# Kernel optimization log

Hardware: AMD Instinct MI355X
Metric: run time of the kernel (lower is better)

## Reference

```python
import jax, jax.numpy as jnp
import numpy as np

B, T, N, D, H = 4, 8, 128, 256, 8
DH = D // H
SH_HID = 16
NUM_FEATS = 3
NUM_COEFF = 4  # l=0 (1) + l=1 (3)
Y0_CONST = 0.28209479177387814   # 1/(2*sqrt(pi)), e3nn 'integral' norm
Y1_CONST = 0.4886025119029199    # sqrt(3/(4*pi))


def setup_inputs() -> dict:
    key = jax.random.key(0)
    ks = jax.random.split(key, 16)
    rn = lambda k, shape, s=1.0: jax.random.normal(k, shape, dtype=jnp.float32) * s
    return {
        "x_0": rn(ks[0], (B, T, N, D)),
        "v_0": rn(ks[1], (B, T, N, D)),
        "concatenated_features": rn(ks[2], (B, T, N, D)),
        "q_data": rn(ks[3], (B, T, N, D)),
        "mask": jnp.ones((B, 1, N, 1), dtype=bool),
        "Wq": rn(ks[4], (D, D), 0.02), "bq": jnp.zeros((D,), jnp.float32),
        "Wkv": rn(ks[5], (NUM_FEATS, D, 2 * D), 0.02),
        "bkv": jnp.zeros((NUM_FEATS, 2 * D), jnp.float32),
        "Wo": rn(ks[6], (D, D), 0.02), "bo": jnp.zeros((D,), jnp.float32),
        "feature_weights": rn(ks[7], (NUM_FEATS,), 0.1),
        "attention_denom": jnp.full((H,), float(DH), dtype=jnp.float32),
        "sh_W1": rn(ks[8], (NUM_COEFF, SH_HID), 0.3), "sh_b1": jnp.zeros((SH_HID,), jnp.float32),
        "sh_W2": rn(ks[9], (SH_HID, SH_HID), 0.3), "sh_b2": jnp.zeros((SH_HID,), jnp.float32),
        "sh_W3": rn(ks[10], (SH_HID, H), 0.3), "sh_b3": jnp.zeros((H,), jnp.float32),
    }


def _rope(t, mask, T_, N_):
    # t: [B,H,S,dh]; time-only RoPE, groups of N_ nodes share a timestep. offset=0.
    B_, H_, S, dh = t.shape
    half = dh // 2
    freqs = 1.0 / (1000.0 ** (2.0 * jnp.arange(half, dtype=jnp.float32) / dh))  # [half]
    pos = jnp.repeat(jnp.arange(T_, dtype=jnp.float32), N_)  # [S]
    angle = pos[:, None] * freqs[None, :]  # [S, half]
    mask_seq = jnp.broadcast_to(mask, (B_, T_, N_, 1)).reshape(B_, 1, S, 1)
    cos_t = jnp.where(mask_seq, jnp.cos(angle)[None, None], 1.0)  # [B,1,S,half]
    sin_t = jnp.where(mask_seq, jnp.sin(angle)[None, None], 0.0)
    t1, t2 = t[..., 0::2], t[..., 1::2]
    return jnp.stack([t1 * cos_t - t2 * sin_t, t1 * sin_t + t2 * cos_t], axis=-1).reshape(t.shape)


def _sh_bias(coords, W1, b1, W2, b2, W3, b3):
    # coords: [B,S,3] -> bias [B,H,S,S]
    rel = coords[:, :, None, :] - coords[:, None, :, :]  # [B,S,S,3]
    norm = jnp.sqrt(jnp.sum(rel * rel, axis=-1, keepdims=True))
    u = rel / (norm + 1e-6)
    Y0 = jnp.full(u.shape[:-1] + (1,), Y0_CONST, dtype=u.dtype)
    Y1 = Y1_CONST * u[..., jnp.array([1, 2, 0])]  # e3nn l=1 order (y,z,x)
    sh = jnp.concatenate([Y0, Y1], axis=-1)  # [B,S,S,4]
    h = jax.nn.silu(sh @ W1 + b1)
    h = jax.nn.silu(h @ W2 + b2)
    bias = h @ W3 + b3  # [B,S,S,H]
    return jnp.transpose(bias, (0, 3, 1, 2))


def reference(x_0, v_0, concatenated_features, q_data, mask,
              Wq, bq, Wkv, bkv, Wo, bo, feature_weights, attention_denom,
              sh_W1, sh_b1, sh_W2, sh_b2, sh_W3, sh_b3):
    B_, T_, N_, D_ = q_data.shape
    S = T_ * N_
    H_ = attention_denom.shape[0]
    dh = D_ // H_

    q = (q_data.reshape(B_, S, D_) @ Wq + bq).reshape(B_, S, H_, dh).transpose(0, 2, 1, 3)
    q = _rope(q, mask, T_, N_)

    coords = x_0[..., :3].reshape(B_, S, 3)
    bias = _sh_bias(coords, sh_W1, sh_b1, sh_W2, sh_b2, sh_W3, sh_b3)  # [B,H,S,S]

    key_mask = jnp.broadcast_to(mask, (B_, T_, N_, 1)).reshape(B_, 1, 1, S)
    gates = jax.nn.softmax(feature_weights)

    out_sum = jnp.zeros_like(q)
    for i, feat in enumerate((x_0, v_0, concatenated_features)):
        kv = feat.reshape(B_, S, D_) @ Wkv[i] + bkv[i]  # [B,S,2D]
        k = kv[..., :D_].reshape(B_, S, H_, dh).transpose(0, 2, 1, 3)
        v = kv[..., D_:].reshape(B_, S, H_, dh).transpose(0, 2, 1, 3)
        k = _rope(k, mask, T_, N_)
        scores = jnp.einsum('bhqd,bhkd->bhqk', q, k) / attention_denom[None, :, None, None]
        scores = scores + bias
        scores = jnp.where(key_mask, scores, -1e9)
        attn = jax.nn.softmax(scores, axis=-1)
        out_sum = out_sum + gates[i] * jnp.einsum('bhqk,bhkd->bhqd', attn, v)

    out = out_sum.transpose(0, 2, 1, 3).reshape(B_, S, D_) @ Wo + bo  # [B,S,D]
    return out.reshape(B_ * T_, N_, D_)
```

## Files before the change

### kernel.cpp

```cpp
#include <hip/hip_runtime.h>
#include <hip/hip_bf16.h>
#include <math.h>


typedef __bf16 bf16;
typedef __attribute__((ext_vector_type(8))) __bf16 bf16x8;
typedef __attribute__((ext_vector_type(4))) __bf16 bf16x4;
typedef __attribute__((ext_vector_type(4))) float  f32x4;

#define MFMA16(a,b,c) __builtin_amdgcn_mfma_f32_16x16x32_bf16((a),(b),(c),0,0,0)
#define FRCP(x) __builtin_amdgcn_rcpf(x)

__device__ __forceinline__ unsigned pk2(float a, float b){
  bf16 x = (bf16)a, y = (bf16)b;
  unsigned short ux = __builtin_bit_cast(unsigned short, x);
  unsigned short uy = __builtin_bit_cast(unsigned short, y);
  return (unsigned)ux | ((unsigned)uy << 16);
}

__global__ __launch_bounds__(256) void proj_kernel(
    const float* __restrict__ x0, const float* __restrict__ v0,
    const float* __restrict__ cf, const float* __restrict__ qd,
    const float* __restrict__ Wq, const float* __restrict__ bq,
    const float* __restrict__ Wkv, const float* __restrict__ bkv,
    const float* __restrict__ dn,
    bf16* __restrict__ Qb, bf16* __restrict__ Kb, bf16* __restrict__ Vtb)
{
  const int mtc = blockIdx.x;
  const int znt = blockIdx.y;
  int z, nt;
  if (znt < 4){ z = 0; nt = znt; } else { z = 1 + ((znt-4)>>3); nt = (znt-4)&7; }

  const float* A; const float* W; const float* bias; int ldw;
  if (z == 0){ A = qd; W = Wq; bias = bq; ldw = 256; }
  else {
    A = (z==1) ? x0 : (z==2) ? v0 : cf;
    W = Wkv + (size_t)(z-1)*256*512;
    bias = bkv + (size_t)(z-1)*512;
    ldw = 512;
  }

  __shared__ alignas(16) bf16 lds_w[64*264];
  __shared__ alignas(16) bf16 ostg[4][1152];
  const int t  = threadIdx.x;
  const int n0 = nt*64;

  {
    int c4 = t & 15, kr = t >> 4;
    #pragma unroll
    for (int i=0;i<16;i++){
      int k = kr + i*16;
      float4 v = *(const float4*)(W + (size_t)k*ldw + n0 + c4*4);
      lds_w[(c4*4+0)*264 + k] = (bf16)v.x;
      lds_w[(c4*4+1)*264 + k] = (bf16)v.y;
      lds_w[(c4*4+2)*264 + k] = (bf16)v.z;
      lds_w[(c4*4+3)*264 + k] = (bf16)v.w;
    }
  }
  __syncthreads();

  const int w = t>>6, lane = t&63, lrow = lane&15, g = lane>>4;
  const f32x4 zf = {0.f,0.f,0.f,0.f};
  const bool isV = (z>0) && (nt>=4);

  const float Cln = 0.43172239f;
  const float fr_e = __expf(-Cln * (float)(lrow>>1));
  const float fr_o = __expf(-Cln * (float)(8 + (lrow>>1)));
  float rs0 = 1.f, rs1 = 1.f;
  if (z==0){ rs0 = 1.f/dn[(nt*2)&7]; rs1 = 1.f/dn[(nt*2+1)&7]; }

  for (int mi=0; mi<4; mi++){
    const int mt = mtc*4 + mi;
    const float* Arow = A + (size_t)(mt*64 + w*16 + lrow)*256;

    f32x4 acc[4] = {zf,zf,zf,zf};
    #pragma unroll
    for (int ks=0;ks<8;ks++){
      float4 a0 = *(const float4*)(Arow + ks*32 + g*8);
      float4 a1 = *(const float4*)(Arow + ks*32 + g*8 + 4);
      bf16x8 af = {(bf16)a0.x,(bf16)a0.y,(bf16)a0.z,(bf16)a0.w,
                   (bf16)a1.x,(bf16)a1.y,(bf16)a1.z,(bf16)a1.w};
      #pragma unroll
      for (int n4=0;n4<4;n4++){
        bf16x8 bb = *(const bf16x8*)(lds_w + (n4*16+lrow)*264 + ks*32 + g*8);
        acc[n4] = MFMA16(af, bb, acc[n4]);
      }
    }

    if (!isV){
      const float tpos = (float)((mt>>1)&7);
      float ae = tpos*fr_e, ao = tpos*fr_o;
      float cs_e = __cosf(ae), sn_e = __sinf(ae);
      float cs_o = __cosf(ao), sn_o = __sinf(ao);
      #pragma unroll
      for (int n4=0;n4<4;n4++){
        int gcol = n0 + n4*16 + lrow;
        float bv = bias[gcol];
        float cs = (n4&1)? cs_o : cs_e;
        float sn = (n4&1)? sn_o : sn_e;
        float rs = (n4>>1)? rs1 : rs0;
        #pragma unroll
        for (int rr=0;rr<4;rr++){
          float v = acc[n4][rr] + bv;
          float p = __shfl_xor(v, 1);
          float o = (lrow&1) ? (p*sn + v*cs) : (v*cs - p*sn);
          o *= rs;
          ostg[w][(g*4+rr)*72 + n4*16 + lrow] = (bf16)o;
        }
      }
      asm volatile("s_waitcnt lgkmcnt(0)" ::: "memory");
      int row = lane>>2, c8 = lane&3;
      int srow = mt*64 + w*16 + row;
      int bb = srow>>10, s = srow&1023;
      #pragma unroll
      for (int hh=0; hh<2; hh++){
        bf16x8 val = *(const bf16x8*)(ostg[w] + row*72 + hh*32 + c8*8);
        int h = (nt*2 + hh)&7;
        bf16* dst = (z==0) ? (Qb + ((size_t)(bb*8+h)*1024 + s)*32 + c8*8)
                           : (Kb + ((size_t)(((z-1)*4+bb)*8+h)*1024 + s)*32 + c8*8);
        *(bf16x8*)dst = val;
      }
    } else {
      #pragma unroll
      for (int n4=0;n4<4;n4++){
        int gcol = n0 + n4*16 + lrow;
        float bv = bias[gcol];
        int hd = gcol - 256; int h = hd>>5, d = hd&31;
        int grow0 = mt*64 + w*16 + g*4;
        int bb = grow0>>10, s0 = grow0&1023;
        int s0p = (s0 & ~31) | (((s0>>2)&3)<<3) | (((s0>>4)&1)<<2);
        bf16x4 pk;
        #pragma unroll
        for (int rr=0;rr<4;rr++) pk[rr] = (bf16)(acc[n4][rr] + bv);
        *(bf16x4*)(Vtb + (((size_t)((z-1)*4+bb)*8 + h)*32 + d)*1024 + s0p) = pk;
      }
    }
  }
}

__global__ __launch_bounds__(512, 2) void attn_kernel(
    const bf16* __restrict__ Qb, const bf16* __restrict__ Kb, const bf16* __restrict__ Vtb,
    const float* __restrict__ x0, const float* __restrict__ fw,
    const float* __restrict__ W1, const float* __restrict__ b1,
    const float* __restrict__ W2, const float* __restrict__ b2,
    const float* __restrict__ W3, const float* __restrict__ b3,
    const float* __restrict__ Wo, const float* __restrict__ bo,
    float* __restrict__ out)
{
  const int bid = blockIdx.x;
  const int xcd = bid & 7;
  const int b   = xcd >> 1;
  const int qt  = (xcd & 1)*32 + (bid >> 3);
  const int q0  = qt*16;
  const int t = threadIdx.x, w = t>>6, lane = t&63, lrow = lane&15, g = lane>>4;

  __shared__ float smem[11776];
  float* ckA = smem;
  bf16* biasT0 = (bf16*)(smem + 3072);

  bf16x8 w1f, w2f, w3f;
  #pragma unroll
  for (int j=0;j<8;j++){
    w1f[j] = (g==0 && j<4)   ? (bf16)W1[j*16 + lrow]       : (bf16)0.f;
    w2f[j] = (j<4)           ? (bf16)W2[(4*g+j)*16 + lrow] : (bf16)0.f;
    w3f[j] = (j<4 && lrow<8) ? (bf16)W3[(4*g+j)*8 + lrow]  : (bf16)0.f;
  }
  float b1r[4], b2r[4], b3r[4];
  #pragma unroll
  for (int rr=0;rr<4;rr++){
    b1r[rr] = b1[g*4+rr];
    b2r[rr] = b2[g*4+rr];
    b3r[rr] = (g<2) ? b3[g*4+rr] : 0.f;
  }

  float f0=fw[0], f1=fw[1], f2=fw[2];
  float fm = fmaxf(f0, fmaxf(f1,f2));
  float e0=__expf(f0-fm), e1=__expf(f1-fm), e2=__expf(f2-fm);
  float ei = FRCP(e0+e1+e2);
  float gate[3] = {e0*ei, e1*ei, e2*ei};

  bf16x8 qf = *(const bf16x8*)(Qb + (((size_t)(b*8+w)*1024) + q0 + lrow)*32 + g*8);

  #pragma unroll
  for (int u=0;u<2;u++){
    int key = u*512 + t;
    const float* src = x0 + ((size_t)b*1024 + key)*256;
    ckA[key*3+0] = src[0]; ckA[key*3+1] = src[1]; ckA[key*3+2] = src[2];
  }
  __syncthreads();
  const float cqx = ckA[(q0+lrow)*3+0], cqy = ckA[(q0+lrow)*3+1], cqz = ckA[(q0+lrow)*3+2];

  auto MLP = [&](int kt_){
    const int k0 = kt_*64;
    bf16* bT = biasT0 + (kt_&1)*8704;
    const f32x4 zf = {0.f,0.f,0.f,0.f};
    #pragma unroll
    for (int m8=0;m8<8;m8++){
      const int m = w*8 + m8;
      float rx = cqx - ckA[(k0+m)*3+0];
      float ry = cqy - ckA[(k0+m)*3+1];
      float rz = cqz - ckA[(k0+m)*3+2];
      float inv = FRCP(__builtin_amdgcn_sqrtf(rx*rx+ry*ry+rz*rz) + 1e-6f);
      bf16x8 shf;
      #pragma unroll
      for (int j=0;j<8;j++) shf[j] = (bf16)0.f;
      if (g==0){
        shf[0] = (bf16)0.28209479177387814f;
        shf[1] = (bf16)(0.4886025119029199f*ry*inv);
        shf[2] = (bf16)(0.4886025119029199f*rz*inv);
        shf[3] = (bf16)(0.4886025119029199f*rx*inv);
      }
      f32x4 c1 = MFMA16(w1f, shf, zf);
      bf16x8 h1f;
      #pragma unroll
      for (int rr=0;rr<4;rr++){
        float hv = c1[rr] + b1r[rr];
        hv = hv * FRCP(1.f + __expf(-hv));
        bf16 hb = (bf16)hv;
        h1f[rr] = hb; h1f[rr+4] = hb;
      }
      f32x4 c2 = MFMA16(w2f, h1f, zf);
      bf16x8 h2f;
      #pragma unroll
      for (int rr=0;rr<4;rr++){
        float hv = c2[rr] + b2r[rr];
        hv = hv * FRCP(1.f + __expf(-hv));
        bf16 hb = (bf16)hv;
        h2f[rr] = hb; h2f[rr+4] = hb;
      }
      f32x4 c3 = MFMA16(w3f, h2f, zf);
      if (g < 2){
        #pragma unroll
        for (int rr=0;rr<4;rr++)
          bT[((g*4+rr)*64 + m)*17 + lrow] = (bf16)(c3[rr] + b3r[rr]);
      }
    }
  };

  float l_run[3] = {0.f,0.f,0.f};
  const f32x4 zf = {0.f,0.f,0.f,0.f};
  f32x4 acc[3][2];
  #pragma unroll
  for (int i=0;i<3;i++){ acc[i][0] = zf; acc[i][1] = zf; }

  MLP(0);
  __syncthreads();

  for (int kt=0;kt<16;kt++){
    const int k0 = kt*64;

    bf16x8 kpre[3][4], vpre[3][2][2];
    #pragma unroll
    for (int i=0;i<3;i++){
      const bf16* Kbase = Kb + ((size_t)(i*4+b)*8 + w)*1024*32;
      #pragma unroll
      for (int k16=0;k16<4;k16++)
        kpre[i][k16] = *(const bf16x8*)(Kbase + (size_t)(k0 + k16*16 + lrow)*32 + g*8);
      const bf16* Vbase = Vtb + ((size_t)(i*4+b)*8 + w)*32*1024;
      #pragma unroll
      for (int dt=0;dt<2;dt++){
        vpre[i][dt][0] = *(const bf16x8*)(Vbase + (size_t)(dt*16+lrow)*1024 + k0      + g*8);
        vpre[i][dt][1] = *(const bf16x8*)(Vbase + (size_t)(dt*16+lrow)*1024 + k0 + 32 + g*8);
      }
    }
    __builtin_amdgcn_sched_barrier(0);

    const bf16* bTr = biasT0 + (kt&1)*8704;
    float bias_r[4][4];
    #pragma unroll
    for (int k16=0;k16<4;k16++)
      #pragma unroll
      for (int rr=0;rr<4;rr++)
        bias_r[k16][rr] = (float)bTr[(w*64 + k16*16 + g*4 + rr)*17 + lrow];

    if (kt < 15) MLP(kt+1);

    #pragma unroll
    for (int i=0;i<3;i++){
      float p[4][4];
      float lp[4];
      #pragma unroll
      for (int k16=0;k16<4;k16++){
        f32x4 sc = MFMA16(kpre[i][k16], qf, zf);
        float s0 = 0.f;
        #pragma unroll
        for (int rr=0;rr<4;rr++){
          float pv = __expf(sc[rr] + bias_r[k16][rr]);
          p[k16][rr] = pv;
          s0 += pv;
        }
        lp[k16] = s0;
      }
      l_run[i] += (lp[0]+lp[1]) + (lp[2]+lp[3]);
      bf16x8 pf0, pf1;
      #pragma unroll
      for (int j=0;j<8;j++){
        pf0[j] = (bf16)p[(j>>2)][j&3];
        pf1[j] = (bf16)p[2+(j>>2)][j&3];
      }
      #pragma unroll
      for (int dt=0;dt<2;dt++){
        acc[i][dt] = MFMA16(vpre[i][dt][0], pf0, acc[i][dt]);
        acc[i][dt] = MFMA16(vpre[i][dt][1], pf1, acc[i][dt]);
      }
    }
    __syncthreads();
  }

  float linv[3];
  #pragma unroll
  for (int i=0;i<3;i++){
    float l = l_run[i];
    l += __shfl_xor(l, 16);
    l += __shfl_xor(l, 32);
    linv[i] = gate[i]*FRCP(l);
  }
  f32x4 o[2];
  #pragma unroll
  for (int dt=0;dt<2;dt++)
    #pragma unroll
    for (int rr=0;rr<4;rr++)
      o[dt][rr] = acc[0][dt][rr]*linv[0] + acc[1][dt][rr]*linv[1] + acc[2][dt][rr]*linv[2];

  unsigned* osTp = (unsigned*)smem;
  __syncthreads();
  #pragma unroll
  for (int dt=0;dt<2;dt++){
    int pb = w*16 + dt*8 + g*2;
    osTp[(pb+0)*17 + lrow] = pk2(o[dt][0], o[dt][1]);
    osTp[(pb+1)*17 + lrow] = pk2(o[dt][2], o[dt][3]);
  }
  __syncthreads();

  #pragma unroll
  for (int nt2=0;nt2<2;nt2++){
    const int n0 = w*32 + nt2*16;
    f32x4 c = zf;
    #pragma unroll
    for (int kb=0;kb<8;kb++){
      bf16x8 af;
      #pragma unroll
      for (int j=0;j<8;j++)
        af[j] = (bf16)Wo[(size_t)(kb*32 + g*8 + j)*256 + n0 + lrow];
      union { unsigned u[4]; bf16x8 v; } bu;
      #pragma unroll
      for (int jj=0;jj<4;jj++)
        bu.u[jj] = osTp[(kb*16 + g*4 + jj)*17 + lrow];
      c = MFMA16(af, bu.v, c);
    }
    #pragma unroll
    for (int rr=0;rr<4;rr++){
      int n = n0 + g*4 + rr;
      out[(size_t)(b*1024 + q0 + lrow)*256 + n] = c[rr] + bo[n];
    }
  }
}

extern "C" void kernel_launch(void* const* d_in, const int* in_sizes, int n_in,
                              void* d_out, int out_size, void* d_ws, size_t ws_size,
                              hipStream_t stream)
{
  (void)in_sizes; (void)n_in; (void)out_size; (void)ws_size;
  const float* x0 = (const float*)d_in[0];
  const float* v0 = (const float*)d_in[1];
  const float* cf = (const float*)d_in[2];
  const float* qd = (const float*)d_in[3];
  const float* Wq = (const float*)d_in[5];
  const float* bq = (const float*)d_in[6];
  const float* Wkv= (const float*)d_in[7];
  const float* bkv= (const float*)d_in[8];
  const float* Wo = (const float*)d_in[9];
  const float* bo = (const float*)d_in[10];
  const float* fw = (const float*)d_in[11];
  const float* dn = (const float*)d_in[12];
  const float* W1 = (const float*)d_in[13];
  const float* b1 = (const float*)d_in[14];
  const float* W2 = (const float*)d_in[15];
  const float* b2 = (const float*)d_in[16];
  const float* W3 = (const float*)d_in[17];
  const float* b3 = (const float*)d_in[18];

  const size_t nQ = (size_t)4*8*1024*32;
  const size_t nK = (size_t)3*4*8*1024*32;
  bf16*  Qb   = (bf16*)d_ws;
  bf16*  Kb   = Qb + nQ;
  bf16*  Vtb  = Kb + nK;
  float* outp = (float*)d_out;

  hipLaunchKernelGGL(proj_kernel, dim3(16,28), dim3(256), 0, stream,
                     x0, v0, cf, qd, Wq, bq, Wkv, bkv, dn, Qb, Kb, Vtb);
  hipLaunchKernelGGL(attn_kernel, dim3(256), dim3(512), 0, stream,
                     Qb, Kb, Vtb, x0, fw, W1,b1,W2,b2,W3,b3, Wo, bo, outp);
}
```

Measured before the change: 240.3 us.

## Split attention key range across two wave groups in 1024-thread blocks

The attention block grows from 512 to 1024 threads. Two groups of 8 waves each process half of the 1024 keys, and their partial accumulators and row sums are merged through shared memory before the output projection, which now uses all 16 waves. K/V register prefetch before the sched barrier is dropped in favour of loads inline with the MFMAs. This raises per-CU parallelism and halves the serial key loop, at the cost of more shared memory, extra barriers and a merge step, and may expose load latency now that prefetching is gone.

After: 315.1 us. +31.1%, slower.

```diff
diff --git a/kernel.cpp b/kernel.cpp
--- a/kernel.cpp
+++ b/kernel.cpp
@@ -138,7 +138,7 @@
   }
 }
 
-__global__ __launch_bounds__(512, 2) void attn_kernel(
+__global__ __launch_bounds__(1024, 4) void attn_kernel(
     const bf16* __restrict__ Qb, const bf16* __restrict__ Kb, const bf16* __restrict__ Vtb,
     const float* __restrict__ x0, const float* __restrict__ fw,
     const float* __restrict__ W1, const float* __restrict__ b1,
@@ -152,11 +152,14 @@
   const int b   = xcd >> 1;
   const int qt  = (xcd & 1)*32 + (bid >> 3);
   const int q0  = qt*16;
-  const int t = threadIdx.x, w = t>>6, lane = t&63, lrow = lane&15, g = lane>>4;
-
-  __shared__ float smem[11776];
+  const int t = threadIdx.x;
+  const int w16 = t>>6, split = w16>>3, w = w16&7;
+  const int lane = t&63, lrow = lane&15, g = lane>>4;
+  const int kbase = split*512;
+
+  __shared__ float smem[20480];
   float* ckA = smem;
-  bf16* biasT0 = (bf16*)(smem + 3072);
+  bf16* bgrp = (bf16*)(smem + 3072) + split*17408;
 
   bf16x8 w1f, w2f, w3f;
   #pragma unroll
@@ -181,18 +184,16 @@
 
   bf16x8 qf = *(const bf16x8*)(Qb + (((size_t)(b*8+w)*1024) + q0 + lrow)*32 + g*8);
 
-  #pragma unroll
-  for (int u=0;u<2;u++){
-    int key = u*512 + t;
-    const float* src = x0 + ((size_t)b*1024 + key)*256;
-    ckA[key*3+0] = src[0]; ckA[key*3+1] = src[1]; ckA[key*3+2] = src[2];
+  {
+    const float* src = x0 + ((size_t)b*1024 + t)*256;
+    ckA[t*3+0] = src[0]; ckA[t*3+1] = src[1]; ckA[t*3+2] = src[2];
   }
   __syncthreads();
   const float cqx = ckA[(q0+lrow)*3+0], cqy = ckA[(q0+lrow)*3+1], cqz = ckA[(q0+lrow)*3+2];
 
   auto MLP = [&](int kt_){
-    const int k0 = kt_*64;
-    bf16* bT = biasT0 + (kt_&1)*8704;
+    const int k0 = kbase + kt_*64;
+    bf16* bT = bgrp + (kt_&1)*8704;
     const f32x4 zf = {0.f,0.f,0.f,0.f};
     #pragma unroll
     for (int m8=0;m8<8;m8++){
@@ -246,42 +247,28 @@
   MLP(0);
   __syncthreads();
 
-  for (int kt=0;kt<16;kt++){
-    const int k0 = kt*64;
-
-    bf16x8 kpre[3][4], vpre[3][2][2];
+  for (int kt=0;kt<8;kt++){
+    const int kg = kbase + kt*64;
+
+    const bf16* bTr = bgrp + (kt&1)*8704;
+    float bias_r[4][4];
+    #pragma unroll
+    for (int k16=0;k16<4;k16++)
+      #pragma unroll
+      for (int rr=0;rr<4;rr++)
+        bias_r[k16][rr] = (float)bTr[(w*64 + k16*16 + g*4 + rr)*17 + lrow];
+
+    if (kt < 7) MLP(kt+1);
+
     #pragma unroll
     for (int i=0;i<3;i++){
       const bf16* Kbase = Kb + ((size_t)(i*4+b)*8 + w)*1024*32;
-      #pragma unroll
-      for (int k16=0;k16<4;k16++)
-        kpre[i][k16] = *(const bf16x8*)(Kbase + (size_t)(k0 + k16*16 + lrow)*32 + g*8);
-      const bf16* Vbase = Vtb + ((size_t)(i*4+b)*8 + w)*32*1024;
-      #pragma unroll
-      for (int dt=0;dt<2;dt++){
-        vpre[i][dt][0] = *(const bf16x8*)(Vbase + (size_t)(dt*16+lrow)*1024 + k0      + g*8);
-        vpre[i][dt][1] = *(const bf16x8*)(Vbase + (size_t)(dt*16+lrow)*1024 + k0 + 32 + g*8);
-      }
-    }
-    __builtin_amdgcn_sched_barrier(0);
-
-    const bf16* bTr = biasT0 + (kt&1)*8704;
-    float bias_r[4][4];
-    #pragma unroll
-    for (int k16=0;k16<4;k16++)
-      #pragma unroll
-      for (int rr=0;rr<4;rr++)
-        bias_r[k16][rr] = (float)bTr[(w*64 + k16*16 + g*4 + rr)*17 + lrow];
-
-    if (kt < 15) MLP(kt+1);
-
-    #pragma unroll
-    for (int i=0;i<3;i++){
       float p[4][4];
       float lp[4];
       #pragma unroll
       for (int k16=0;k16<4;k16++){
-        f32x4 sc = MFMA16(kpre[i][k16], qf, zf);
+        bf16x8 kf = *(const bf16x8*)(Kbase + (size_t)(kg + k16*16 + lrow)*32 + g*8);
+        f32x4 sc = MFMA16(kf, qf, zf);
         float s0 = 0.f;
         #pragma unroll
         for (int rr=0;rr<4;rr++){
@@ -298,43 +285,71 @@
         pf0[j] = (bf16)p[(j>>2)][j&3];
         pf1[j] = (bf16)p[2+(j>>2)][j&3];
       }
+      const bf16* Vbase = Vtb + ((size_t)(i*4+b)*8 + w)*32*1024;
       #pragma unroll
       for (int dt=0;dt<2;dt++){
-        acc[i][dt] = MFMA16(vpre[i][dt][0], pf0, acc[i][dt]);
-        acc[i][dt] = MFMA16(vpre[i][dt][1], pf1, acc[i][dt]);
+        bf16x8 vf0 = *(const bf16x8*)(Vbase + (size_t)(dt*16+lrow)*1024 + kg      + g*8);
+        bf16x8 vf1 = *(const bf16x8*)(Vbase + (size_t)(dt*16+lrow)*1024 + kg + 32 + g*8);
+        acc[i][dt] = MFMA16(vf0, pf0, acc[i][dt]);
+        acc[i][dt] = MFMA16(vf1, pf1, acc[i][dt]);
       }
     }
     __syncthreads();
   }
 
-  float linv[3];
-  #pragma unroll
-  for (int i=0;i<3;i++){
-    float l = l_run[i];
-    l += __shfl_xor(l, 16);
-    l += __shfl_xor(l, 32);
-    linv[i] = gate[i]*FRCP(l);
-  }
+  if (split == 1){
+    float* mb = smem + (w*64 + lane)*28;
+    #pragma unroll
+    for (int i=0;i<3;i++){
+      #pragma unroll
+      for (int dt=0;dt<2;dt++)
+        #pragma unroll
+        for (int rr=0;rr<4;rr++) mb[i*8 + dt*4 + rr] = acc[i][dt][rr];
+      mb[24+i] = l_run[i];
+    }
+  }
+  __syncthreads();
+
   f32x4 o[2];
-  #pragma unroll
-  for (int dt=0;dt<2;dt++)
-    #pragma unroll
-    for (int rr=0;rr<4;rr++)
-      o[dt][rr] = acc[0][dt][rr]*linv[0] + acc[1][dt][rr]*linv[1] + acc[2][dt][rr]*linv[2];
+  if (split == 0){
+    float* mb = smem + (w*64 + lane)*28;
+    #pragma unroll
+    for (int i=0;i<3;i++){
+      #pragma unroll
+      for (int dt=0;dt<2;dt++)
+        #pragma unroll
+        for (int rr=0;rr<4;rr++) acc[i][dt][rr] += mb[i*8 + dt*4 + rr];
+      l_run[i] += mb[24+i];
+    }
+    float linv[3];
+    #pragma unroll
+    for (int i=0;i<3;i++){
+      float l = l_run[i];
+      l += __shfl_xor(l, 16);
+      l += __shfl_xor(l, 32);
+      linv[i] = gate[i]*FRCP(l);
+    }
+    #pragma unroll
+    for (int dt=0;dt<2;dt++)
+      #pragma unroll
+      for (int rr=0;rr<4;rr++)
+        o[dt][rr] = acc[0][dt][rr]*linv[0] + acc[1][dt][rr]*linv[1] + acc[2][dt][rr]*linv[2];
+  }
+  __syncthreads();
 
   unsigned* osTp = (unsigned*)smem;
-  __syncthreads();
-  #pragma unroll
-  for (int dt=0;dt<2;dt++){
-    int pb = w*16 + dt*8 + g*2;
-    osTp[(pb+0)*17 + lrow] = pk2(o[dt][0], o[dt][1]);
-    osTp[(pb+1)*17 + lrow] = pk2(o[dt][2], o[dt][3]);
-  }
-  __syncthreads();
-
-  #pragma unroll
-  for (int nt2=0;nt2<2;nt2++){
-    const int n0 = w*32 + nt2*16;
+  if (split == 0){
+    #pragma unroll
+    for (int dt=0;dt<2;dt++){
+      int pb = w*16 + dt*8 + g*2;
+      osTp[(pb+0)*17 + lrow] = pk2(o[dt][0], o[dt][1]);
+      osTp[(pb+1)*17 + lrow] = pk2(o[dt][2], o[dt][3]);
+    }
+  }
+  __syncthreads();
+
+  {
+    const int n0 = w16*16;
     f32x4 c = zf;
     #pragma unroll
     for (int kb=0;kb<8;kb++){
@@ -389,6 +404,6 @@
 
   hipLaunchKernelGGL(proj_kernel, dim3(16,28), dim3(256), 0, stream,
                      x0, v0, cf, qd, Wq, bq, Wkv, bkv, dn, Qb, Kb, Vtb);
-  hipLaunchKernelGGL(attn_kernel, dim3(256), dim3(512), 0, stream,
+  hipLaunchKernelGGL(attn_kernel, dim3(256), dim3(1024), 0, stream,
                      Qb, Kb, Vtb, x0, fw, W1,b1,W2,b2,W3,b3, Wo, bo, outp);
 }
```
